# Kernel optimization log

Measured on AMD Instinct MI355X. Metric: run time of the kernel, lower is better.

## Reference

```python
import jax, jax.numpy as jnp
import numpy as np

TWO_PI = 2.0 * np.pi
LN_EPS = 1e-5


def _periods(out_dim, nb):
    # periods[i,j,g] = i*(out_dim*nb) + j*nb + g + 2
    return jnp.arange(out_dim * out_dim * nb, dtype=jnp.float32).reshape(out_dim, out_dim, nb) + 2.0


def _layer(x, M, gamma, beta, P, residual):
    # x: (B,S,in), M: (out,in), P: (out,out,nb)
    out_dim, _, nb = P.shape
    S = x.shape[1]
    xt = jnp.matmul(x, M.T)  # (B,S,out)
    mu = jnp.mean(xt, axis=-1, keepdims=True)
    var = jnp.mean((xt - mu) ** 2, axis=-1, keepdims=True)
    xn = (xt - mu) / jnp.sqrt(var + LN_EPS) * gamma + beta
    pos = jnp.arange(S, dtype=jnp.float32)[:, None, None, None]  # (S,1,1,1)
    phi = jnp.cos(TWO_PI * pos / _periods(out_dim, nb)[None])  # (S,out,out,nb)
    W = jnp.einsum('ijg,sijg->sij', P, phi)  # (S,out,out) contract basis first
    Nk = jnp.einsum('bsj,sij->bsi', xn, W)  # (B,S,out)
    return Nk + residual


def setup_inputs() -> dict:
    key = jax.random.key(0)
    ks = jax.random.split(key, 8)
    B, S, D_in, D, NB = 8, 1024, 64, 96, 8
    u = lambda k, shape, a: jax.random.uniform(k, shape, jnp.float32, -a, a)
    return {
        'seq': jax.random.normal(ks[0], (B, S, D_in), jnp.float32),
        'M1': u(ks[1], (D, D_in), 0.5),
        'P1': u(ks[2], (D, D, NB), 0.1),
        'Wres1': u(ks[3], (D, D_in), 0.1),
        'g1': jnp.ones((D,), jnp.float32),
        'b1': jnp.zeros((D,), jnp.float32),
        'M2': u(ks[4], (D, D), 0.5),
        'P2': u(ks[5], (D, D, NB), 0.1),
        'g2': jnp.ones((D,), jnp.float32),
        'b2': jnp.zeros((D,), jnp.float32),
    }


def reference(seq, M1, P1, Wres1, g1, b1, M2, P2, g2, b2):
    # Layer 1: 64 -> 96, 'separate' residual uses a Linear projection
    x1 = _layer(seq, M1, g1, b1, P1, jnp.matmul(seq, Wres1.T))
    # Layer 2: 96 -> 96, 'separate' residual with in_dim==out_dim is Identity
    x2 = _layer(x1, M2, g2, b2, P2, x1)
    return x2
```

## Files before the change

kernel.cpp:

```cpp
#include <hip/hip_runtime.h>
#include <hip/hip_fp16.h>

#define S_LEN    1024
#define B_SZ     8
#define D_IN     64
#define D_OUT    96
#define NB       8
#define NE       (D_OUT * D_OUT)
#define CHUNK    8
#define NCHUNK   (S_LEN / CHUNK)
#define SPAD     100
#define XPAD     68
#define HPAD     104
#define NT_MAIN  512
#define NT_W     256

__device__ __forceinline__ float cos_rev(float v) {
    v -= floorf(v);
    return __builtin_amdgcn_cosf(v);
}

__global__ void __launch_bounds__(NT_W)
w_kernel(const float* __restrict__ P1, const float* __restrict__ P2,
         __half* __restrict__ W1, __half* __restrict__ W2) {
    const int c  = blockIdx.x / (NE / NT_W);
    const int eb = blockIdx.x % (NE / NT_W);
    const int e  = eb * NT_W + threadIdx.x;
    const int s0 = c * CHUNK;
    const float s0f = (float)s0;

    float p1l[NB], p2l[NB];
    *(float4*)&p1l[0] = *(const float4*)(P1 + e * NB);
    *(float4*)&p1l[4] = *(const float4*)(P1 + e * NB + 4);
    *(float4*)&p2l[0] = *(const float4*)(P2 + e * NB);
    *(float4*)&p2l[4] = *(const float4*)(P2 + e * NB + 4);

    float cc[NB], cp[NB], kk[NB];
    #pragma unroll
    for (int g = 0; g < NB; ++g) {
        const float inv = __builtin_amdgcn_rcpf((float)(e * NB + 2 + g));
        cc[g] = cos_rev(s0f * inv);
        cp[g] = cos_rev((s0f - 1.0f) * inv);
        kk[g] = 2.0f * __builtin_amdgcn_cosf(inv);
    }

    #pragma unroll
    for (int s = s0; s < s0 + CHUNK; ++s) {
        float a1 = 0.0f, a2 = 0.0f;
        #pragma unroll
        for (int g = 0; g < NB; ++g) {
            a1 = fmaf(p1l[g], cc[g], a1);
            a2 = fmaf(p2l[g], cc[g], a2);
        }
        W1[s * NE + e] = __float2half(a1);
        W2[s * NE + e] = __float2half(a2);
        #pragma unroll
        for (int g = 0; g < NB; ++g) {
            float cn = fmaf(kk[g], cc[g], -cp[g]);
            cp[g] = cc[g];
            cc[g] = cn;
        }
    }
}

__device__ __forceinline__ void block_layernorm_w64(float* __restrict__ buf,
                                                    const float* __restrict__ gamma,
                                                    const float* __restrict__ beta,
                                                    int tid) {
    const int b    = tid >> 6;
    const int lane = tid & 63;
    float* row = buf + b * SPAD;
    const bool hi = (lane < 32);
    float v0 = row[lane];
    float v1 = hi ? row[lane + 64] : 0.0f;
    float sum = v0 + v1;
    float sq  = fmaf(v0, v0, v1 * v1);
    #pragma unroll
    for (int off = 32; off > 0; off >>= 1) {
        sum += __shfl_down(sum, off, 64);
        sq  += __shfl_down(sq,  off, 64);
    }
    sum = __shfl(sum, 0, 64);
    sq  = __shfl(sq,  0, 64);
    const float mu  = sum * (1.0f / 96.0f);
    const float var = fmaf(sq, 1.0f / 96.0f, -(mu * mu));
    const float rs  = rsqrtf(var + 1e-5f);
    row[lane] = fmaf((v0 - mu) * rs, gamma[lane], beta[lane]);
    if (hi)
        row[lane + 64] = fmaf((v1 - mu) * rs, gamma[lane + 64], beta[lane + 64]);
}

__device__ __forceinline__ float nk_dot(const __half* __restrict__ wrow,
                                        const float* __restrict__ xr) {
    float acc = 0.0f;
    #pragma unroll
    for (int h = 0; h < 2; ++h) {
        #pragma unroll
        for (int j = h * 6; j < h * 6 + 6; ++j) {
            float4 raw = *(const float4*)(wrow + 8 * j);
            const __half2* hp = (const __half2*)&raw;
            float2 c0 = __half22float2(hp[0]);
            float2 c1 = __half22float2(hp[1]);
            float2 c2 = __half22float2(hp[2]);
            float2 c3 = __half22float2(hp[3]);
            float4 xv0 = *(const float4*)(xr + 8 * j);
            float4 xv1 = *(const float4*)(xr + 8 * j + 4);
            acc = fmaf(c0.x, xv0.x, acc); acc = fmaf(c0.y, xv0.y, acc);
            acc = fmaf(c1.x, xv0.z, acc); acc = fmaf(c1.y, xv0.w, acc);
            acc = fmaf(c2.x, xv1.x, acc); acc = fmaf(c2.y, xv1.y, acc);
            acc = fmaf(c3.x, xv1.z, acc); acc = fmaf(c3.y, xv1.w, acc);
        }
    }
    return acc;
}

__device__ __forceinline__ void stage_W(__half* __restrict__ wh,
                                        const __half* __restrict__ Wg,
                                        int tid) {
    for (int cidx = tid; cidx < NE / 8; cidx += NT_MAIN) {
        const int i = cidx / 12;
        const int j = (cidx % 12) * 8;
        *(float4*)(wh + i * HPAD + j) = *(const float4*)(Wg + cidx * 8);
    }
}

__global__ void __launch_bounds__(NT_MAIN, 4)
hier_main(const float* __restrict__ seq,  const float* __restrict__ M1,
          const float* __restrict__ Wres1, const float* __restrict__ g1,
          const float* __restrict__ b1,   const float* __restrict__ M2,
          const float* __restrict__ g2,   const float* __restrict__ b2,
          const __half* __restrict__ W1g, const __half* __restrict__ W2g,
          float* __restrict__ out) {
    __shared__ __align__(16) __half wh [D_OUT * HPAD];
    __shared__ __align__(16) float xin[B_SZ * XPAD];
    __shared__ __align__(16) float xn [B_SZ * SPAD];
    __shared__ __align__(16) float x1b[B_SZ * SPAD];

    const int s   = blockIdx.x;
    const int tid = threadIdx.x;

    {
        int b = tid >> 6, k = tid & 63;
        xin[b * XPAD + k] = seq[(b * S_LEN + s) * D_IN + k];
    }
    stage_W(wh, W1g + (size_t)s * NE, tid);
    __syncthreads();

    for (int idx = tid; idx < B_SZ * D_OUT; idx += NT_MAIN) {
        int i = idx >> 3, b = idx & 7;
        const float4* m  = (const float4*)(M1 + i * D_IN);
        const float4* wr = (const float4*)(Wres1 + i * D_IN);
        const float*  xr = xin + b * XPAD;
        float at = 0.0f, ar = 0.0f;
        #pragma unroll
        for (int k = 0; k < D_IN / 4; ++k) {
            float4 mv = m[k], rv = wr[k];
            float x0 = xr[4*k], x1 = xr[4*k+1], x2 = xr[4*k+2], x3 = xr[4*k+3];
            at = fmaf(mv.x, x0, fmaf(mv.y, x1, fmaf(mv.z, x2, fmaf(mv.w, x3, at))));
            ar = fmaf(rv.x, x0, fmaf(rv.y, x1, fmaf(rv.z, x2, fmaf(rv.w, x3, ar))));
        }
        xn [b * SPAD + i] = at;
        x1b[b * SPAD + i] = ar;
    }
    __syncthreads();

    block_layernorm_w64(xn, g1, b1, tid);
    __syncthreads();

    for (int idx = tid; idx < B_SZ * D_OUT; idx += NT_MAIN) {
        int i = idx >> 3, b = idx & 7;
        x1b[b * SPAD + i] += nk_dot(wh + i * HPAD, xn + b * SPAD);
    }
    __syncthreads();

    stage_W(wh, W2g + (size_t)s * NE, tid);

    for (int idx = tid; idx < B_SZ * D_OUT; idx += NT_MAIN) {
        int i = idx >> 3, b = idx & 7;
        const float4* m  = (const float4*)(M2 + i * D_OUT);
        const float*  xr = x1b + b * SPAD;
        float at = 0.0f;
        #pragma unroll
        for (int k = 0; k < D_OUT / 4; ++k) {
            float4 mv = m[k];
            at = fmaf(mv.x, xr[4*k], fmaf(mv.y, xr[4*k+1],
                 fmaf(mv.z, xr[4*k+2], fmaf(mv.w, xr[4*k+3], at))));
        }
        xn[b * SPAD + i] = at;
    }
    __syncthreads();

    block_layernorm_w64(xn, g2, b2, tid);
    __syncthreads();

    for (int idx = tid; idx < B_SZ * D_OUT; idx += NT_MAIN) {
        int i = idx >> 3, b = idx & 7;
        float acc = nk_dot(wh + i * HPAD, xn + b * SPAD);
        out[(b * S_LEN + s) * D_OUT + i] = acc + x1b[b * SPAD + i];
    }
}

__global__ void __launch_bounds__(NT_W)
hier_fallback(const float* __restrict__ seq,  const float* __restrict__ M1,
              const float* __restrict__ P1,   const float* __restrict__ Wres1,
              const float* __restrict__ g1,   const float* __restrict__ b1,
              const float* __restrict__ M2,   const float* __restrict__ P2,
              const float* __restrict__ g2,   const float* __restrict__ b2,
              float* __restrict__ out) {
    __shared__ __align__(16) float w[D_OUT * SPAD];
    __shared__ __align__(16) float xin[B_SZ * XPAD];
    __shared__ __align__(16) float xn [B_SZ * SPAD];
    __shared__ __align__(16) float x1b[B_SZ * SPAD];
    const int s = blockIdx.x, tid = threadIdx.x;
    const float sf = (float)s;

    for (int idx = tid; idx < B_SZ * D_IN; idx += NT_W) {
        int b = idx >> 6, k = idx & (D_IN - 1);
        xin[b * XPAD + k] = seq[(b * S_LEN + s) * D_IN + k];
    }
    for (int e = tid; e < NE; e += NT_W) {
        float pl[8];
        *(float4*)&pl[0] = *(const float4*)(P1 + e * NB);
        *(float4*)&pl[4] = *(const float4*)(P1 + e * NB + 4);
        float acc = 0.0f;
        #pragma unroll
        for (int g = 0; g < NB; ++g) {
            float v = sf * __builtin_amdgcn_rcpf((float)(e * NB + 2 + g));
            acc = fmaf(pl[g], cos_rev(v), acc);
        }
        int i = e / D_OUT;
        w[e + (SPAD - D_OUT) * i] = acc;
    }
    __syncthreads();
    for (int idx = tid; idx < B_SZ * D_OUT; idx += NT_W) {
        int i = idx >> 3, b = idx & 7;
        const float4* m  = (const float4*)(M1 + i * D_IN);
        const float4* wr = (const float4*)(Wres1 + i * D_IN);
        const float*  xr = xin + b * XPAD;
        float at = 0.0f, ar = 0.0f;
        #pragma unroll
        for (int k = 0; k < D_IN / 4; ++k) {
            float4 mv = m[k], rv = wr[k];
            float x0 = xr[4*k], x1 = xr[4*k+1], x2 = xr[4*k+2], x3 = xr[4*k+3];
            at = fmaf(mv.x, x0, fmaf(mv.y, x1, fmaf(mv.z, x2, fmaf(mv.w, x3, at))));
            ar = fmaf(rv.x, x0, fmaf(rv.y, x1, fmaf(rv.z, x2, fmaf(rv.w, x3, ar))));
        }
        xn [b * SPAD + i] = at;
        x1b[b * SPAD + i] = ar;
    }
    __syncthreads();
    {
        const int b = tid >> 5, r = tid & 31;
        float* row = xn + b * SPAD;
        float v0 = row[r], v1 = row[r + 32], v2 = row[r + 64];
        float sum = v0 + v1 + v2, sq = fmaf(v0, v0, fmaf(v1, v1, v2 * v2));
        #pragma unroll
        for (int off = 16; off > 0; off >>= 1) {
            sum += __shfl_down(sum, off, 32);
            sq  += __shfl_down(sq,  off, 32);
        }
        sum = __shfl(sum, 0, 32); sq = __shfl(sq, 0, 32);
        float mu = sum * (1.0f/96.0f), var = fmaf(sq, 1.0f/96.0f, -(mu*mu));
        float rs = rsqrtf(var + 1e-5f);
        row[r]      = fmaf((v0 - mu) * rs, g1[r],      b1[r]);
        row[r + 32] = fmaf((v1 - mu) * rs, g1[r + 32], b1[r + 32]);
        row[r + 64] = fmaf((v2 - mu) * rs, g1[r + 64], b1[r + 64]);
    }
    __syncthreads();
    for (int idx = tid; idx < B_SZ * D_OUT; idx += NT_W) {
        int i = idx >> 3, b = idx & 7;
        const float* wrow = w + i * SPAD;
        const float* xr   = xn + b * SPAD;
        float acc = 0.0f;
        #pragma unroll
        for (int j = 0; j < D_OUT / 4; ++j) {
            float4 wv = *(const float4*)(wrow + 4 * j);
            float4 xv = *(const float4*)(xr + 4 * j);
            acc = fmaf(wv.x, xv.x, fmaf(wv.y, xv.y, fmaf(wv.z, xv.z, fmaf(wv.w, xv.w, acc))));
        }
        x1b[b * SPAD + i] += acc;
    }
    __syncthreads();
    for (int e = tid; e < NE; e += NT_W) {
        float pl[8];
        *(float4*)&pl[0] = *(const float4*)(P2 + e * NB);
        *(float4*)&pl[4] = *(const float4*)(P2 + e * NB + 4);
        float acc = 0.0f;
        #pragma unroll
        for (int g = 0; g < NB; ++g) {
            float v = sf * __builtin_amdgcn_rcpf((float)(e * NB + 2 + g));
            acc = fmaf(pl[g], cos_rev(v), acc);
        }
        int i = e / D_OUT;
        w[e + (SPAD - D_OUT) * i] = acc;
    }
    for (int idx = tid; idx < B_SZ * D_OUT; idx += NT_W) {
        int i = idx >> 3, b = idx & 7;
        const float4* m  = (const float4*)(M2 + i * D_OUT);
        const float*  xr = x1b + b * SPAD;
        float at = 0.0f;
        #pragma unroll
        for (int k = 0; k < D_OUT / 4; ++k) {
            float4 mv = m[k];
            at = fmaf(mv.x, xr[4*k], fmaf(mv.y, xr[4*k+1],
                 fmaf(mv.z, xr[4*k+2], fmaf(mv.w, xr[4*k+3], at))));
        }
        xn[b * SPAD + i] = at;
    }
    __syncthreads();
    {
        const int b = tid >> 5, r = tid & 31;
        float* row = xn + b * SPAD;
        float v0 = row[r], v1 = row[r + 32], v2 = row[r + 64];
        float sum = v0 + v1 + v2, sq = fmaf(v0, v0, fmaf(v1, v1, v2 * v2));
        #pragma unroll
        for (int off = 16; off > 0; off >>= 1) {
            sum += __shfl_down(sum, off, 32);
            sq  += __shfl_down(sq,  off, 32);
        }
        sum = __shfl(sum, 0, 32); sq = __shfl(sq, 0, 32);
        float mu = sum * (1.0f/96.0f), var = fmaf(sq, 1.0f/96.0f, -(mu*mu));
        float rs = rsqrtf(var + 1e-5f);
        row[r]      = fmaf((v0 - mu) * rs, g2[r],      b2[r]);
        row[r + 32] = fmaf((v1 - mu) * rs, g2[r + 32], b2[r + 32]);
        row[r + 64] = fmaf((v2 - mu) * rs, g2[r + 64], b2[r + 64]);
    }
    __syncthreads();
    for (int idx = tid; idx < B_SZ * D_OUT; idx += NT_W) {
        int i = idx >> 3, b = idx & 7;
        const float* wrow = w + i * SPAD;
        const float* xr   = xn + b * SPAD;
        float acc = 0.0f;
        #pragma unroll
        for (int j = 0; j < D_OUT / 4; ++j) {
            float4 wv = *(const float4*)(wrow + 4 * j);
            float4 xv = *(const float4*)(xr + 4 * j);
            acc = fmaf(wv.x, xv.x, fmaf(wv.y, xv.y, fmaf(wv.z, xv.z, fmaf(wv.w, xv.w, acc))));
        }
        out[(b * S_LEN + s) * D_OUT + i] = acc + x1b[b * SPAD + i];
    }
}

extern "C" void kernel_launch(void* const* d_in, const int* in_sizes, int n_in,
                              void* d_out, int out_size, void* d_ws, size_t ws_size,
                              hipStream_t stream) {
    const float* seq   = (const float*)d_in[0];
    const float* M1    = (const float*)d_in[1];
    const float* P1    = (const float*)d_in[2];
    const float* Wres1 = (const float*)d_in[3];
    const float* g1    = (const float*)d_in[4];
    const float* b1    = (const float*)d_in[5];
    const float* M2    = (const float*)d_in[6];
    const float* P2    = (const float*)d_in[7];
    const float* g2    = (const float*)d_in[8];
    const float* b2    = (const float*)d_in[9];
    float* out = (float*)d_out;

    const size_t need = (size_t)2 * S_LEN * NE * sizeof(__half);
    if (ws_size >= need) {
        __half* W1 = (__half*)d_ws;
        __half* W2 = W1 + (size_t)S_LEN * NE;
        w_kernel<<<dim3(NCHUNK * (NE / NT_W)), dim3(NT_W), 0, stream>>>(P1, P2, W1, W2);
        hier_main<<<dim3(S_LEN), dim3(NT_MAIN), 0, stream>>>(
            seq, M1, Wres1, g1, b1, M2, g2, b2, W1, W2, out);
    } else {
        hier_fallback<<<dim3(S_LEN), dim3(NT_W), 0, stream>>>(
            seq, M1, P1, Wres1, g1, b1, M2, P2, g2, b2, out);
    }
}
```

Before: 125.3 us.

## Move layer-1 input projections into producer kernel and streamline per-position consumer

The first-layer input projection and residual projection (seq·M1ᵀ, seq·Wres1ᵀ) move out of the per-position main kernel into the W-producing kernel as extra blocks, written to workspace XT/RS buffers. The consumer kernel stages both W1 and W2 tiles into shared memory up front. Each wave then handles one batch row with per-lane output columns, doing layernorm in registers via shuffles and removing most block-wide barriers. The cost is extra global traffic for XT/RS, larger shared memory per block, and a larger workspace requirement. Intra-wave shared-memory reads of xr after writes also rely on wave-level execution ordering rather than explicit syncs.

```diff
diff --git a/kernel.cpp b/kernel.cpp
--- a/kernel.cpp
+++ b/kernel.cpp
@@ -9,198 +9,234 @@
 #define NE       (D_OUT * D_OUT)
 #define CHUNK    8
 #define NCHUNK   (S_LEN / CHUNK)
+#define NT_P     256
+#define NWBLK    (NCHUNK * (NE / NT_P))
+#define GROWS    32
+#define NROWS    (B_SZ * S_LEN)
+#define NGBLK    (NROWS / GROWS)
+#define WPITCH   104
+#define NT_C     512
 #define SPAD     100
 #define XPAD     68
-#define HPAD     104
-#define NT_MAIN  512
-#define NT_W     256
 
 __device__ __forceinline__ float cos_rev(float v) {
     v -= floorf(v);
     return __builtin_amdgcn_cosf(v);
 }
 
-__global__ void __launch_bounds__(NT_W)
-w_kernel(const float* __restrict__ P1, const float* __restrict__ P2,
-         __half* __restrict__ W1, __half* __restrict__ W2) {
-    const int c  = blockIdx.x / (NE / NT_W);
-    const int eb = blockIdx.x % (NE / NT_W);
-    const int e  = eb * NT_W + threadIdx.x;
-    const int s0 = c * CHUNK;
-    const float s0f = (float)s0;
-
-    float p1l[NB], p2l[NB];
-    *(float4*)&p1l[0] = *(const float4*)(P1 + e * NB);
-    *(float4*)&p1l[4] = *(const float4*)(P1 + e * NB + 4);
-    *(float4*)&p2l[0] = *(const float4*)(P2 + e * NB);
-    *(float4*)&p2l[4] = *(const float4*)(P2 + e * NB + 4);
-
-    float cc[NB], cp[NB], kk[NB];
+__global__ void __launch_bounds__(NT_P)
+producer(const float* __restrict__ P1, const float* __restrict__ P2,
+         const float* __restrict__ seq, const float* __restrict__ M1,
+         const float* __restrict__ Wres1,
+         __half* __restrict__ W1, __half* __restrict__ W2,
+         float* __restrict__ XT, float* __restrict__ RS) {
+    const int tid = threadIdx.x;
+    if (blockIdx.x < NWBLK) {
+        const int c  = blockIdx.x / (NE / NT_P);
+        const int eb = blockIdx.x % (NE / NT_P);
+        const int e  = eb * NT_P + tid;
+        const int s0 = c * CHUNK;
+        const float s0f = (float)s0;
+
+        float p1l[NB], p2l[NB];
+        *(float4*)&p1l[0] = *(const float4*)(P1 + e * NB);
+        *(float4*)&p1l[4] = *(const float4*)(P1 + e * NB + 4);
+        *(float4*)&p2l[0] = *(const float4*)(P2 + e * NB);
+        *(float4*)&p2l[4] = *(const float4*)(P2 + e * NB + 4);
+
+        float cc[NB], cp[NB], kk[NB];
+        #pragma unroll
+        for (int g = 0; g < NB; ++g) {
+            const float inv = __builtin_amdgcn_rcpf((float)(e * NB + 2 + g));
+            cc[g] = cos_rev(s0f * inv);
+            cp[g] = cos_rev((s0f - 1.0f) * inv);
+            kk[g] = 2.0f * __builtin_amdgcn_cosf(inv);
+        }
+        #pragma unroll
+        for (int s = s0; s < s0 + CHUNK; ++s) {
+            float a1 = 0.0f, a2 = 0.0f;
+            #pragma unroll
+            for (int g = 0; g < NB; ++g) {
+                a1 = fmaf(p1l[g], cc[g], a1);
+                a2 = fmaf(p2l[g], cc[g], a2);
+            }
+            W1[s * NE + e] = __float2half(a1);
+            W2[s * NE + e] = __float2half(a2);
+            #pragma unroll
+            for (int g = 0; g < NB; ++g) {
+                float cn = fmaf(kk[g], cc[g], -cp[g]);
+                cp[g] = cc[g];
+                cc[g] = cn;
+            }
+        }
+    } else {
+        __shared__ __align__(16) float xs[GROWS * XPAD];
+        const int r0 = (blockIdx.x - NWBLK) * GROWS;
+        for (int cdx = tid; cdx < GROWS * (D_IN / 4); cdx += NT_P) {
+            int rr = cdx >> 4, q = cdx & 15;
+            *(float4*)(xs + rr * XPAD + q * 4) =
+                *(const float4*)(seq + (size_t)(r0 + rr) * D_IN + q * 4);
+        }
+        __syncthreads();
+        const int rr = tid >> 3;
+        const int ig = tid & 7;
+        const float* xr = xs + rr * XPAD;
+        #pragma unroll
+        for (int ii = 0; ii < 12; ++ii) {
+            const int i = ig + ii * 8;
+            const float4* m = (const float4*)(M1 + i * D_IN);
+            const float4* w = (const float4*)(Wres1 + i * D_IN);
+            float at = 0.0f, ar = 0.0f;
+            #pragma unroll
+            for (int k = 0; k < D_IN / 4; ++k) {
+                float4 mv = m[k], rv = w[k];
+                float4 xv = *(const float4*)(xr + 4 * k);
+                at = fmaf(mv.x, xv.x, fmaf(mv.y, xv.y, fmaf(mv.z, xv.z, fmaf(mv.w, xv.w, at))));
+                ar = fmaf(rv.x, xv.x, fmaf(rv.y, xv.y, fmaf(rv.z, xv.z, fmaf(rv.w, xv.w, ar))));
+            }
+            XT[(size_t)(r0 + rr) * D_OUT + i] = at;
+            RS[(size_t)(r0 + rr) * D_OUT + i] = ar;
+        }
+    }
+}
+
+__device__ __forceinline__ float nkdot(const __half* __restrict__ wrow,
+                                       const float* __restrict__ xr) {
+    float acc = 0.0f;
     #pragma unroll
-    for (int g = 0; g < NB; ++g) {
-        const float inv = __builtin_amdgcn_rcpf((float)(e * NB + 2 + g));
-        cc[g] = cos_rev(s0f * inv);
-        cp[g] = cos_rev((s0f - 1.0f) * inv);
-        kk[g] = 2.0f * __builtin_amdgcn_cosf(inv);
-    }
-
-    #pragma unroll
-    for (int s = s0; s < s0 + CHUNK; ++s) {
-        float a1 = 0.0f, a2 = 0.0f;
-        #pragma unroll
-        for (int g = 0; g < NB; ++g) {
-            a1 = fmaf(p1l[g], cc[g], a1);
-            a2 = fmaf(p2l[g], cc[g], a2);
-        }
-        W1[s * NE + e] = __float2half(a1);
-        W2[s * NE + e] = __float2half(a2);
-        #pragma unroll
-        for (int g = 0; g < NB; ++g) {
-            float cn = fmaf(kk[g], cc[g], -cp[g]);
-            cp[g] = cc[g];
-            cc[g] = cn;
-        }
-    }
-}
-
-__device__ __forceinline__ void block_layernorm_w64(float* __restrict__ buf,
-                                                    const float* __restrict__ gamma,
-                                                    const float* __restrict__ beta,
-                                                    int tid) {
-    const int b    = tid >> 6;
-    const int lane = tid & 63;
-    float* row = buf + b * SPAD;
-    const bool hi = (lane < 32);
-    float v0 = row[lane];
-    float v1 = hi ? row[lane + 64] : 0.0f;
-    float sum = v0 + v1;
-    float sq  = fmaf(v0, v0, v1 * v1);
-    #pragma unroll
-    for (int off = 32; off > 0; off >>= 1) {
-        sum += __shfl_down(sum, off, 64);
-        sq  += __shfl_down(sq,  off, 64);
-    }
-    sum = __shfl(sum, 0, 64);
-    sq  = __shfl(sq,  0, 64);
-    const float mu  = sum * (1.0f / 96.0f);
-    const float var = fmaf(sq, 1.0f / 96.0f, -(mu * mu));
-    const float rs  = rsqrtf(var + 1e-5f);
-    row[lane] = fmaf((v0 - mu) * rs, gamma[lane], beta[lane]);
-    if (hi)
-        row[lane + 64] = fmaf((v1 - mu) * rs, gamma[lane + 64], beta[lane + 64]);
-}
-
-__device__ __forceinline__ float nk_dot(const __half* __restrict__ wrow,
+    for (int j = 0; j < 12; ++j) {
+        float4 raw = *(const float4*)(wrow + 8 * j);
+        const __half2* hp = (const __half2*)&raw;
+        float2 c0 = __half22float2(hp[0]);
+        float2 c1 = __half22float2(hp[1]);
+        float2 c2 = __half22float2(hp[2]);
+        float2 c3 = __half22float2(hp[3]);
+        float4 x0 = *(const float4*)(xr + 8 * j);
+        float4 x1 = *(const float4*)(xr + 8 * j + 4);
+        acc = fmaf(c0.x, x0.x, acc); acc = fmaf(c0.y, x0.y, acc);
+        acc = fmaf(c1.x, x0.z, acc); acc = fmaf(c1.y, x0.w, acc);
+        acc = fmaf(c2.x, x1.x, acc); acc = fmaf(c2.y, x1.y, acc);
+        acc = fmaf(c3.x, x1.z, acc); acc = fmaf(c3.y, x1.w, acc);
+    }
+    return acc;
+}
+
+__device__ __forceinline__ float gemv96(const float* __restrict__ mrow,
                                         const float* __restrict__ xr) {
     float acc = 0.0f;
     #pragma unroll
-    for (int h = 0; h < 2; ++h) {
-        #pragma unroll
-        for (int j = h * 6; j < h * 6 + 6; ++j) {
-            float4 raw = *(const float4*)(wrow + 8 * j);
-            const __half2* hp = (const __half2*)&raw;
-            float2 c0 = __half22float2(hp[0]);
-            float2 c1 = __half22float2(hp[1]);
-            float2 c2 = __half22float2(hp[2]);
-            float2 c3 = __half22float2(hp[3]);
-            float4 xv0 = *(const float4*)(xr + 8 * j);
-            float4 xv1 = *(const float4*)(xr + 8 * j + 4);
-            acc = fmaf(c0.x, xv0.x, acc); acc = fmaf(c0.y, xv0.y, acc);
-            acc = fmaf(c1.x, xv0.z, acc); acc = fmaf(c1.y, xv0.w, acc);
-            acc = fmaf(c2.x, xv1.x, acc); acc = fmaf(c2.y, xv1.y, acc);
-            acc = fmaf(c3.x, xv1.z, acc); acc = fmaf(c3.y, xv1.w, acc);
-        }
+    for (int k = 0; k < 24; ++k) {
+        float4 mv = *(const float4*)(mrow + 4 * k);
+        float4 xv = *(const float4*)(xr + 4 * k);
+        acc = fmaf(mv.x, xv.x, fmaf(mv.y, xv.y, fmaf(mv.z, xv.z, fmaf(mv.w, xv.w, acc))));
     }
     return acc;
 }
 
-__device__ __forceinline__ void stage_W(__half* __restrict__ wh,
-                                        const __half* __restrict__ Wg,
-                                        int tid) {
-    for (int cidx = tid; cidx < NE / 8; cidx += NT_MAIN) {
-        const int i = cidx / 12;
-        const int j = (cidx % 12) * 8;
-        *(float4*)(wh + i * HPAD + j) = *(const float4*)(Wg + cidx * 8);
-    }
-}
-
-__global__ void __launch_bounds__(NT_MAIN, 4)
-hier_main(const float* __restrict__ seq,  const float* __restrict__ M1,
-          const float* __restrict__ Wres1, const float* __restrict__ g1,
-          const float* __restrict__ b1,   const float* __restrict__ M2,
-          const float* __restrict__ g2,   const float* __restrict__ b2,
-          const __half* __restrict__ W1g, const __half* __restrict__ W2g,
-          float* __restrict__ out) {
-    __shared__ __align__(16) __half wh [D_OUT * HPAD];
-    __shared__ __align__(16) float xin[B_SZ * XPAD];
-    __shared__ __align__(16) float xn [B_SZ * SPAD];
-    __shared__ __align__(16) float x1b[B_SZ * SPAD];
-
-    const int s   = blockIdx.x;
-    const int tid = threadIdx.x;
+__global__ void __launch_bounds__(NT_C, 4)
+consumer(const float* __restrict__ XT, const float* __restrict__ RS,
+         const float* __restrict__ M2,
+         const float* __restrict__ g1, const float* __restrict__ b1,
+         const float* __restrict__ g2, const float* __restrict__ b2,
+         const __half* __restrict__ W1g, const __half* __restrict__ W2g,
+         float* __restrict__ out) {
+    __shared__ __align__(16) __half wh1[D_OUT * WPITCH];
+    __shared__ __align__(16) __half wh2[D_OUT * WPITCH];
+    __shared__ __align__(16) float  xbuf[B_SZ * SPAD];
+
+    const int s    = blockIdx.x;
+    const int tid  = threadIdx.x;
+    const int b    = tid >> 6;
+    const int lane = tid & 63;
+    const bool lo  = (lane < 32);
 
     {
-        int b = tid >> 6, k = tid & 63;
-        xin[b * XPAD + k] = seq[(b * S_LEN + s) * D_IN + k];
-    }
-    stage_W(wh, W1g + (size_t)s * NE, tid);
-    __syncthreads();
-
-    for (int idx = tid; idx < B_SZ * D_OUT; idx += NT_MAIN) {
-        int i = idx >> 3, b = idx & 7;
-        const float4* m  = (const float4*)(M1 + i * D_IN);
-        const float4* wr = (const float4*)(Wres1 + i * D_IN);
-        const float*  xr = xin + b * XPAD;
-        float at = 0.0f, ar = 0.0f;
-        #pragma unroll
-        for (int k = 0; k < D_IN / 4; ++k) {
-            float4 mv = m[k], rv = wr[k];
-            float x0 = xr[4*k], x1 = xr[4*k+1], x2 = xr[4*k+2], x3 = xr[4*k+3];
-            at = fmaf(mv.x, x0, fmaf(mv.y, x1, fmaf(mv.z, x2, fmaf(mv.w, x3, at))));
-            ar = fmaf(rv.x, x0, fmaf(rv.y, x1, fmaf(rv.z, x2, fmaf(rv.w, x3, ar))));
-        }
-        xn [b * SPAD + i] = at;
-        x1b[b * SPAD + i] = ar;
-    }
-    __syncthreads();
-
-    block_layernorm_w64(xn, g1, b1, tid);
-    __syncthreads();
-
-    for (int idx = tid; idx < B_SZ * D_OUT; idx += NT_MAIN) {
-        int i = idx >> 3, b = idx & 7;
-        x1b[b * SPAD + i] += nk_dot(wh + i * HPAD, xn + b * SPAD);
-    }
-    __syncthreads();
-
-    stage_W(wh, W2g + (size_t)s * NE, tid);
-
-    for (int idx = tid; idx < B_SZ * D_OUT; idx += NT_MAIN) {
-        int i = idx >> 3, b = idx & 7;
-        const float4* m  = (const float4*)(M2 + i * D_OUT);
-        const float*  xr = x1b + b * SPAD;
-        float at = 0.0f;
-        #pragma unroll
-        for (int k = 0; k < D_OUT / 4; ++k) {
-            float4 mv = m[k];
-            at = fmaf(mv.x, xr[4*k], fmaf(mv.y, xr[4*k+1],
-                 fmaf(mv.z, xr[4*k+2], fmaf(mv.w, xr[4*k+3], at))));
-        }
-        xn[b * SPAD + i] = at;
-    }
-    __syncthreads();
-
-    block_layernorm_w64(xn, g2, b2, tid);
-    __syncthreads();
-
-    for (int idx = tid; idx < B_SZ * D_OUT; idx += NT_MAIN) {
-        int i = idx >> 3, b = idx & 7;
-        float acc = nk_dot(wh + i * HPAD, xn + b * SPAD);
-        out[(b * S_LEN + s) * D_OUT + i] = acc + x1b[b * SPAD + i];
-    }
-}
-
-__global__ void __launch_bounds__(NT_W)
+        const __half* W1s = W1g + (size_t)s * NE;
+        const __half* W2s = W2g + (size_t)s * NE;
+        for (int c = tid; c < NE / 8; c += NT_C) {
+            int i = c / 12, j = (c % 12) * 8;
+            *(float4*)(wh1 + i * WPITCH + j) = *(const float4*)(W1s + c * 8);
+        }
+        for (int c = tid; c < NE / 8; c += NT_C) {
+            int i = c / 12, j = (c % 12) * 8;
+            *(float4*)(wh2 + i * WPITCH + j) = *(const float4*)(W2s + c * 8);
+        }
+    }
+
+    const size_t r = (size_t)b * S_LEN + s;
+    float xt0 = XT[r * D_OUT + lane];
+    float rs0 = RS[r * D_OUT + lane];
+    float xt1 = 0.0f, rs1 = 0.0f;
+    if (lo) {
+        xt1 = XT[r * D_OUT + 64 + lane];
+        rs1 = RS[r * D_OUT + 64 + lane];
+    }
+    __syncthreads();
+
+    float* xr = xbuf + b * SPAD;
+
+    {
+        float sum = xt0 + xt1;
+        float sq  = fmaf(xt0, xt0, xt1 * xt1);
+        #pragma unroll
+        for (int off = 32; off > 0; off >>= 1) {
+            sum += __shfl_down(sum, off, 64);
+            sq  += __shfl_down(sq,  off, 64);
+        }
+        sum = __shfl(sum, 0, 64);
+        sq  = __shfl(sq,  0, 64);
+        const float mu  = sum * (1.0f / 96.0f);
+        const float var = fmaf(sq, 1.0f / 96.0f, -(mu * mu));
+        const float rst = rsqrtf(var + 1e-5f);
+        float xn0 = fmaf((xt0 - mu) * rst, g1[lane], b1[lane]);
+        xr[lane] = xn0;
+        if (lo) {
+            float xn1 = fmaf((xt1 - mu) * rst, g1[64 + lane], b1[64 + lane]);
+            xr[64 + lane] = xn1;
+        }
+    }
+
+    float x10 = rs0 + nkdot(wh1 + lane * WPITCH, xr);
+    float x11 = 0.0f;
+    if (lo) x11 = rs1 + nkdot(wh1 + (64 + lane) * WPITCH, xr);
+
+    xr[lane] = x10;
+    if (lo) xr[64 + lane] = x11;
+
+    float t0 = gemv96(M2 + lane * D_OUT, xr);
+    float t1 = 0.0f;
+    if (lo) t1 = gemv96(M2 + (64 + lane) * D_OUT, xr);
+
+    {
+        float sum = t0 + t1;
+        float sq  = fmaf(t0, t0, t1 * t1);
+        #pragma unroll
+        for (int off = 32; off > 0; off >>= 1) {
+            sum += __shfl_down(sum, off, 64);
+            sq  += __shfl_down(sq,  off, 64);
+        }
+        sum = __shfl(sum, 0, 64);
+        sq  = __shfl(sq,  0, 64);
+        const float mu  = sum * (1.0f / 96.0f);
+        const float var = fmaf(sq, 1.0f / 96.0f, -(mu * mu));
+        const float rst = rsqrtf(var + 1e-5f);
+        float xn0 = fmaf((t0 - mu) * rst, g2[lane], b2[lane]);
+        xr[lane] = xn0;
+        if (lo) {
+            float xn1 = fmaf((t1 - mu) * rst, g2[64 + lane], b2[64 + lane]);
+            xr[64 + lane] = xn1;
+        }
+    }
+
+    float o0 = nkdot(wh2 + lane * WPITCH, xr) + x10;
+    out[r * D_OUT + lane] = o0;
+    if (lo) {
+        float o1 = nkdot(wh2 + (64 + lane) * WPITCH, xr) + x11;
+        out[r * D_OUT + 64 + lane] = o1;
+    }
+}
+
+__global__ void __launch_bounds__(NT_P)
 hier_fallback(const float* __restrict__ seq,  const float* __restrict__ M1,
               const float* __restrict__ P1,   const float* __restrict__ Wres1,
               const float* __restrict__ g1,   const float* __restrict__ b1,
@@ -214,11 +250,11 @@
     const int s = blockIdx.x, tid = threadIdx.x;
     const float sf = (float)s;
 
-    for (int idx = tid; idx < B_SZ * D_IN; idx += NT_W) {
+    for (int idx = tid; idx < B_SZ * D_IN; idx += NT_P) {
         int b = idx >> 6, k = idx & (D_IN - 1);
         xin[b * XPAD + k] = seq[(b * S_LEN + s) * D_IN + k];
     }
-    for (int e = tid; e < NE; e += NT_W) {
+    for (int e = tid; e < NE; e += NT_P) {
         float pl[8];
         *(float4*)&pl[0] = *(const float4*)(P1 + e * NB);
         *(float4*)&pl[4] = *(const float4*)(P1 + e * NB + 4);
@@ -232,7 +268,7 @@
         w[e + (SPAD - D_OUT) * i] = acc;
     }
     __syncthreads();
-    for (int idx = tid; idx < B_SZ * D_OUT; idx += NT_W) {
+    for (int idx = tid; idx < B_SZ * D_OUT; idx += NT_P) {
         int i = idx >> 3, b = idx & 7;
         const float4* m  = (const float4*)(M1 + i * D_IN);
         const float4* wr = (const float4*)(Wres1 + i * D_IN);
@@ -250,9 +286,9 @@
     }
     __syncthreads();
     {
-        const int b = tid >> 5, r = tid & 31;
+        const int b = tid >> 5, rr = tid & 31;
         float* row = xn + b * SPAD;
-        float v0 = row[r], v1 = row[r + 32], v2 = row[r + 64];
+        float v0 = row[rr], v1 = row[rr + 32], v2 = row[rr + 64];
         float sum = v0 + v1 + v2, sq = fmaf(v0, v0, fmaf(v1, v1, v2 * v2));
         #pragma unroll
         for (int off = 16; off > 0; off >>= 1) {
@@ -262,12 +298,12 @@
         sum = __shfl(sum, 0, 32); sq = __shfl(sq, 0, 32);
         float mu = sum * (1.0f/96.0f), var = fmaf(sq, 1.0f/96.0f, -(mu*mu));
         float rs = rsqrtf(var + 1e-5f);
-        row[r]      = fmaf((v0 - mu) * rs, g1[r],      b1[r]);
-        row[r + 32] = fmaf((v1 - mu) * rs, g1[r + 32], b1[r + 32]);
-        row[r + 64] = fmaf((v2 - mu) * rs, g1[r + 64], b1[r + 64]);
-    }
-    __syncthreads();
-    for (int idx = tid; idx < B_SZ * D_OUT; idx += NT_W) {
+        row[rr]      = fmaf((v0 - mu) * rs, g1[rr],      b1[rr]);
+        row[rr + 32] = fmaf((v1 - mu) * rs, g1[rr + 32], b1[rr + 32]);
+        row[rr + 64] = fmaf((v2 - mu) * rs, g1[rr + 64], b1[rr + 64]);
+    }
+    __syncthreads();
+    for (int idx = tid; idx < B_SZ * D_OUT; idx += NT_P) {
         int i = idx >> 3, b = idx & 7;
         const float* wrow = w + i * SPAD;
         const float* xr   = xn + b * SPAD;
@@ -281,7 +317,7 @@
         x1b[b * SPAD + i] += acc;
     }
     __syncthreads();
-    for (int e = tid; e < NE; e += NT_W) {
+    for (int e = tid; e < NE; e += NT_P) {
         float pl[8];
         *(float4*)&pl[0] = *(const float4*)(P2 + e * NB);
         *(float4*)&pl[4] = *(const float4*)(P2 + e * NB + 4);
@@ -294,7 +330,7 @@
         int i = e / D_OUT;
         w[e + (SPAD - D_OUT) * i] = acc;
     }
-    for (int idx = tid; idx < B_SZ * D_OUT; idx += NT_W) {
+    for (int idx = tid; idx < B_SZ * D_OUT; idx += NT_P) {
         int i = idx >> 3, b = idx & 7;
         const float4* m  = (const float4*)(M2 + i * D_OUT);
         const float*  xr = x1b + b * SPAD;
@@ -309,9 +345,9 @@
     }
     __syncthreads();
     {
-        const int b = tid >> 5, r = tid & 31;
+        const int b = tid >> 5, rr = tid & 31;
         float* row = xn + b * SPAD;
-        float v0 = row[r], v1 = row[r + 32], v2 = row[r + 64];
+        float v0 = row[rr], v1 = row[rr + 32], v2 = row[rr + 64];
         float sum = v0 + v1 + v2, sq = fmaf(v0, v0, fmaf(v1, v1, v2 * v2));
         #pragma unroll
         for (int off = 16; off > 0; off >>= 1) {
@@ -321,12 +357,12 @@
         sum = __shfl(sum, 0, 32); sq = __shfl(sq, 0, 32);
         float mu = sum * (1.0f/96.0f), var = fmaf(sq, 1.0f/96.0f, -(mu*mu));
         float rs = rsqrtf(var + 1e-5f);
-        row[r]      = fmaf((v0 - mu) * rs, g2[r],      b2[r]);
-        row[r + 32] = fmaf((v1 - mu) * rs, g2[r + 32], b2[r + 32]);
-        row[r + 64] = fmaf((v2 - mu) * rs, g2[r + 64], b2[r + 64]);
-    }
-    __syncthreads();
-    for (int idx = tid; idx < B_SZ * D_OUT; idx += NT_W) {
+        row[rr]      = fmaf((v0 - mu) * rs, g2[rr],      b2[rr]);
+        row[rr + 32] = fmaf((v1 - mu) * rs, g2[rr + 32], b2[rr + 32]);
+        row[rr + 64] = fmaf((v2 - mu) * rs, g2[rr + 64], b2[rr + 64]);
+    }
+    __syncthreads();
+    for (int idx = tid; idx < B_SZ * D_OUT; idx += NT_P) {
         int i = idx >> 3, b = idx & 7;
         const float* wrow = w + i * SPAD;
         const float* xr   = xn + b * SPAD;
@@ -356,15 +392,20 @@
     const float* b2    = (const float*)d_in[9];
     float* out = (float*)d_out;
 
-    const size_t need = (size_t)2 * S_LEN * NE * sizeof(__half);
+    const size_t w_bytes  = (size_t)2 * S_LEN * NE * sizeof(__half);
+    const size_t xt_bytes = (size_t)NROWS * D_OUT * sizeof(float);
+    const size_t need     = w_bytes + 2 * xt_bytes;
     if (ws_size >= need) {
         __half* W1 = (__half*)d_ws;
         __half* W2 = W1 + (size_t)S_LEN * NE;
-        w_kernel<<<dim3(NCHUNK * (NE / NT_W)), dim3(NT_W), 0, stream>>>(P1, P2, W1, W2);
-        hier_main<<<dim3(S_LEN), dim3(NT_MAIN), 0, stream>>>(
-            seq, M1, Wres1, g1, b1, M2, g2, b2, W1, W2, out);
+        float*  XT = (float*)((char*)d_ws + w_bytes);
+        float*  RS = XT + (size_t)NROWS * D_OUT;
+        producer<<<dim3(NWBLK + NGBLK), dim3(NT_P), 0, stream>>>(
+            P1, P2, seq, M1, Wres1, W1, W2, XT, RS);
+        consumer<<<dim3(S_LEN), dim3(NT_C), 0, stream>>>(
+            XT, RS, M2, g1, b1, g2, b2, W1, W2, out);
     } else {
-        hier_fallback<<<dim3(S_LEN), dim3(NT_W), 0, stream>>>(
+        hier_fallback<<<dim3(S_LEN), dim3(NT_P), 0, stream>>>(
             seq, M1, P1, Wres1, g1, b1, M2, P2, g2, b2, out);
     }
 }
```

Result: slower. 258.5 us (+106.2%).
